# Kernel optimization log

Measured on AMD Instinct MI355X. Metric: run time of the kernel, lower is better.

Reference implementation:

```python
import jax, jax.numpy as jnp
import numpy as np
from jax import lax


def setup_inputs() -> dict:
    key = jax.random.key(0)
    k1, k2, k3, k4, k5 = jax.random.split(key, 5)
    B, T, K = 512, 1024, 64
    emissions = jax.random.normal(k1, (B, T, K), dtype=jnp.float32)
    tags = jax.random.randint(k2, (B, T), 0, K).astype(jnp.int64)
    mask = jnp.ones((B, T), dtype=bool)
    # CRF parameters, init uniform(-0.1, 0.1) as in reset_parameters
    transitions = jax.random.uniform(k3, (K, K), minval=-0.1, maxval=0.1, dtype=jnp.float32)
    start_transitions = jax.random.uniform(k4, (K,), minval=-0.1, maxval=0.1, dtype=jnp.float32)
    end_transitions = jax.random.uniform(k5, (K,), minval=-0.1, maxval=0.1, dtype=jnp.float32)
    return {"emissions": emissions, "tags": tags, "mask": mask,
            "transitions": transitions, "start_transitions": start_transitions,
            "end_transitions": end_transitions}


def _log_partition(em, mk, transitions, start_transitions, end_transitions):
    # em: (T, B, K) time-major; mk: (T, B) bool
    def step(score, inp):
        em_t, m_t = inp                     # (B, K), (B,)
        # (B, K_prev, 1) + (K_prev, K_next) + (B, 1, K_next) -> lse over prev
        nxt = jax.nn.logsumexp(score[:, :, None] + transitions[None, :, :]
                               + em_t[:, None, :], axis=1)
        score = jnp.where(m_t[:, None], nxt, score)
        return score, None
    score0 = start_transitions + em[0]      # (B, K)
    score, _ = lax.scan(step, score0, (em[1:], mk[1:]))
    return jax.nn.logsumexp(score + end_transitions, axis=1)  # (B,)


def _gold_score(em, tg, mk, transitions, start_transitions, end_transitions):
    # em: (T, B, K); tg: (T, B) int; mk: (T, B) bool
    T, B, K = em.shape
    mf = mk.astype(em.dtype)
    emis = jnp.take_along_axis(em, tg[:, :, None], axis=2)[:, :, 0]  # (T, B)
    score = start_transitions[tg[0]] + jnp.sum(emis * mf, axis=0)
    trans = transitions[tg[:-1], tg[1:]]                              # (T-1, B)
    score = score + jnp.sum(trans * mf[1:], axis=0)
    last_idx = jnp.sum(mk, axis=0).astype(jnp.int32) - 1
    last_tags = tg[last_idx, jnp.arange(B)]
    return score + end_transitions[last_tags]


def reference(emissions, tags, mask, transitions, start_transitions, end_transitions):
    # batch_first=True -> transpose to time-major (T, B, ...)
    em = jnp.transpose(emissions, (1, 0, 2))
    tg = tags.T
    mk = mask.T
    logZ = _log_partition(em, mk, transitions, start_transitions, end_transitions)
    gold = _gold_score(em, tg, mk, transitions, start_transitions, end_transitions)
    return jnp.mean(logZ - gold)
```

## Files before the change

kernel.cpp:

```cpp
#include <hip/hip_runtime.h>
#include <hip/hip_bf16.h>

#define TT 1024
#define KS 64
#define PFD 8

typedef __attribute__((ext_vector_type(8))) short bf16x8;
typedef __attribute__((ext_vector_type(4))) float f32x4;

__device__ __forceinline__ unsigned short f2bf(float x) {
    union { __hip_bfloat16 h; unsigned short s; } u;
    u.h = __float2bfloat16(x);
    return u.s;
}
__device__ __forceinline__ float bflo(unsigned u) {
    union { unsigned v; float f; } w; w.v = u << 16; return w.f;
}
__device__ __forceinline__ float bfhi(unsigned u) {
    union { unsigned v; float f; } w; w.v = u & 0xFFFF0000u; return w.f;
}
__device__ __forceinline__ unsigned cvtpk(float a, float b) {
    unsigned r;
    asm("v_cvt_pk_bf16_f32 %0, %1, %2" : "=v"(r) : "v"(a), "v"(b));
    return r;
}
__device__ __forceinline__ unsigned pkadd(unsigned a, unsigned b) {
    unsigned r;
    asm("v_pk_add_u16 %0, %1, %2" : "=v"(r) : "v"(a), "v"(b));
    return r;
}

__global__ __launch_bounds__(256) void crf_expem(
    const float* __restrict__ em, uint4* __restrict__ g, long long n8)
{
    long long i = (long long)blockIdx.x * blockDim.x + threadIdx.x;
    const long long stride = (long long)gridDim.x * blockDim.x;
    const float4* p = (const float4*)em;
    for (; i < n8; i += stride) {
        float4 a = p[i * 2], b = p[i * 2 + 1];
        uint4 o;
        o.x = (unsigned)f2bf(__expf(a.x)) | ((unsigned)f2bf(__expf(a.y)) << 16);
        o.y = (unsigned)f2bf(__expf(a.z)) | ((unsigned)f2bf(__expf(a.w)) << 16);
        o.z = (unsigned)f2bf(__expf(b.x)) | ((unsigned)f2bf(__expf(b.y)) << 16);
        o.w = (unsigned)f2bf(__expf(b.z)) | ((unsigned)f2bf(__expf(b.w)) << 16);
        g[i] = o;
    }
}

__global__ __launch_bounds__(64, 1) void crf_logZ_v11(
    const float* __restrict__ em,
    const uint4* __restrict__ g4,
    const int* __restrict__ mask,
    const float* __restrict__ trans,
    const float* __restrict__ startT,
    const float* __restrict__ endT,
    float* __restrict__ logZ)
{
    const int l = threadIdx.x;
    const int c = l & 15;
    const int h = l >> 4;
    const long long b = (long long)blockIdx.x * 16 + c;

    const int sigc = 8 * (c >> 2) + (c & 3);
    bf16x8 E[4][2];
#pragma unroll
    for (int m = 0; m < 4; ++m) {
        const int col = 32 * (m >> 1) + 4 * (m & 1) + sigc;
#pragma unroll
        for (int kk = 0; kk < 2; ++kk) {
            union { unsigned short s[8]; bf16x8 v; } u;
#pragma unroll
            for (int e = 0; e < 8; ++e)
                u.s[e] = f2bf(__expf(trans[(32 * kk + 8 * h + e) * KS + col]));
            E[m][kk] = u.v;
        }
    }

    const long long embase = b * (long long)TT * KS;
    const unsigned long long gp =
        (unsigned long long)(const void*)((const char*)g4 + embase * 2 + h * 16);
    const unsigned long long mp =
        (unsigned long long)(const void*)(mask + b * TT);

    unsigned aw0, aw1, aw2, aw3, aw4, aw5, aw6, aw7;
    {
        const float* erow = em + embase;
        float w0[16];
#pragma unroll
        for (int kk = 0; kk < 2; ++kk)
#pragma unroll
            for (int e = 0; e < 8; ++e) {
                const int j = 32 * kk + 8 * h + e;
                w0[8 * kk + e] = __expf(erow[j] + startT[j]);
            }
        aw0 = cvtpk(w0[0], w0[1]);   aw1 = cvtpk(w0[2], w0[3]);
        aw2 = cvtpk(w0[4], w0[5]);   aw3 = cvtpk(w0[6], w0[7]);
        aw4 = cvtpk(w0[8], w0[9]);   aw5 = cvtpk(w0[10], w0[11]);
        aw6 = cvtpk(w0[12], w0[13]); aw7 = cvtpk(w0[14], w0[15]);
    }
    float M = 0.f;

    uint4 ga[PFD], gc[PFD];
    int   mvp[PFD];
#pragma unroll
    for (int u = 0; u < PFD; ++u) {
        const unsigned long long a  = gp + (unsigned long long)(1 + u) * 128ull;
        const unsigned long long ma = mp + (unsigned long long)(1 + u) * 4ull;
        asm volatile("global_load_dwordx4 %0, %1, off" : "=&v"(ga[u]) : "v"(a));
        asm volatile("global_load_dwordx4 %0, %1, off offset:64" : "=&v"(gc[u]) : "v"(a));
        asm volatile("global_load_dword %0, %1, off" : "=&v"(mvp[u]) : "v"(ma));
    }

    unsigned kadd = 0;
    float    sln2 = 0.f;
#define CRF_CTRL() do {                                                        \
    const unsigned l0 = aw0 & 0xffffu, h0 = aw0 >> 16;                         \
    const unsigned l4 = aw4 & 0xffffu, h4 = aw4 >> 16;                         \
    unsigned um = l0 > h0 ? l0 : h0;                                           \
    um = um > l4 ? um : l4;  um = um > h4 ? um : h4;                           \
    unsigned sx = (unsigned)__shfl_xor((int)um, 16); um = um > sx ? um : sx;   \
    sx = (unsigned)__shfl_xor((int)um, 32);          um = um > sx ? um : sx;   \
    const unsigned k16 = (0x3F80u - (um & 0x7F80u)) & 0xffffu;                 \
    kadd = (k16 << 16) | k16;                                                  \
    sln2 = (float)((int)((um >> 7) & 0xffu) - 127) * 0.693147180559945f;       \
} while (0)

#define CRF_STEP(t, u, APPLY) do {                                             \
    union { unsigned uu[4]; bf16x8 v; } A0, A1;                                \
    A0.uu[0] = aw0; A0.uu[1] = aw1; A0.uu[2] = aw2; A0.uu[3] = aw3;            \
    A1.uu[0] = aw4; A1.uu[1] = aw5; A1.uu[2] = aw6; A1.uu[3] = aw7;            \
    const f32x4 z = {0.f, 0.f, 0.f, 0.f};                                      \
    f32x4 d0 = __builtin_amdgcn_mfma_f32_16x16x32_bf16(E[0][0], A0.v, z,0,0,0);\
    f32x4 d1 = __builtin_amdgcn_mfma_f32_16x16x32_bf16(E[1][0], A0.v, z,0,0,0);\
    f32x4 d2 = __builtin_amdgcn_mfma_f32_16x16x32_bf16(E[2][0], A0.v, z,0,0,0);\
    f32x4 d3 = __builtin_amdgcn_mfma_f32_16x16x32_bf16(E[3][0], A0.v, z,0,0,0);\
    d0 = __builtin_amdgcn_mfma_f32_16x16x32_bf16(E[0][1], A1.v, d0, 0,0,0);    \
    d1 = __builtin_amdgcn_mfma_f32_16x16x32_bf16(E[1][1], A1.v, d1, 0,0,0);    \
    d2 = __builtin_amdgcn_mfma_f32_16x16x32_bf16(E[2][1], A1.v, d2, 0,0,0);    \
    d3 = __builtin_amdgcn_mfma_f32_16x16x32_bf16(E[3][1], A1.v, d3, 0,0,0);    \
    asm volatile("s_waitcnt vmcnt(21)" ::: "memory");                          \
    __builtin_amdgcn_sched_barrier(0);                                         \
    const uint4 v0 = ga[u], v1 = gc[u];                                        \
    const int mvv = ((t) <= TT - 1) ? mvp[u] : 0;                              \
    const float g00 = bflo(v0.x), g01 = bfhi(v0.x);                            \
    const float g02 = bflo(v0.y), g03 = bfhi(v0.y);                            \
    const float g10 = bflo(v0.z), g11 = bfhi(v0.z);                            \
    const float g12 = bflo(v0.w), g13 = bfhi(v0.w);                            \
    const float g20 = bflo(v1.x), g21 = bfhi(v1.x);                            \
    const float g22 = bflo(v1.y), g23 = bfhi(v1.y);                            \
    const float g30 = bflo(v1.z), g31 = bfhi(v1.z);                            \
    const float g32 = bflo(v1.w), g33 = bfhi(v1.w);                            \
    unsigned q0, q1, q2, q3, q4, q5, q6, q7;                                   \
    if (APPLY) {                                                               \
        q0 = pkadd(cvtpk(d0.x * g00, d0.y * g01), kadd);                       \
        q1 = pkadd(cvtpk(d0.z * g02, d0.w * g03), kadd);                       \
        q2 = pkadd(cvtpk(d1.x * g10, d1.y * g11), kadd);                       \
        q3 = pkadd(cvtpk(d1.z * g12, d1.w * g13), kadd);                       \
        q4 = pkadd(cvtpk(d2.x * g20, d2.y * g21), kadd);                       \
        q5 = pkadd(cvtpk(d2.z * g22, d2.w * g23), kadd);                       \
        q6 = pkadd(cvtpk(d3.x * g30, d3.y * g31), kadd);                       \
        q7 = pkadd(cvtpk(d3.z * g32, d3.w * g33), kadd);                       \
    } else {                                                                   \
        q0 = cvtpk(d0.x * g00, d0.y * g01);                                    \
        q1 = cvtpk(d0.z * g02, d0.w * g03);                                    \
        q2 = cvtpk(d1.x * g10, d1.y * g11);                                    \
        q3 = cvtpk(d1.z * g12, d1.w * g13);                                    \
        q4 = cvtpk(d2.x * g20, d2.y * g21);                                    \
        q5 = cvtpk(d2.z * g22, d2.w * g23);                                    \
        q6 = cvtpk(d3.x * g30, d3.y * g31);                                    \
        q7 = cvtpk(d3.z * g32, d3.w * g33);                                    \
    }                                                                          \
    aw0 = mvv ? q0 : aw0; aw1 = mvv ? q1 : aw1;                                \
    aw2 = mvv ? q2 : aw2; aw3 = mvv ? q3 : aw3;                                \
    aw4 = mvv ? q4 : aw4; aw5 = mvv ? q5 : aw5;                                \
    aw6 = mvv ? q6 : aw6; aw7 = mvv ? q7 : aw7;                                \
    if (APPLY) { M = mvv ? (M + sln2) : M; }                                   \
    {                                                                          \
        const int tn = ((t) + PFD <= TT - 1) ? ((t) + PFD) : (TT - 1);         \
        const unsigned long long a  = gp + (unsigned long long)tn * 128ull;    \
        const unsigned long long ma = mp + (unsigned long long)tn * 4ull;      \
        asm volatile("global_load_dwordx4 %0, %1, off" : "=&v"(ga[u]) : "v"(a)); \
        asm volatile("global_load_dwordx4 %0, %1, off offset:64" : "=&v"(gc[u]) : "v"(a)); \
        asm volatile("global_load_dword %0, %1, off" : "=&v"(mvp[u]) : "v"(ma)); \
    }                                                                          \
} while (0)

    for (int t0 = 1; t0 < TT + 1; t0 += PFD) {
        CRF_STEP(t0 + 0, 0, 0);
        CRF_CTRL();
        CRF_STEP(t0 + 1, 1, 0);
        CRF_STEP(t0 + 2, 2, 1);
        CRF_STEP(t0 + 3, 3, 0);
        CRF_STEP(t0 + 4, 4, 0);
        CRF_CTRL();
        CRF_STEP(t0 + 5, 5, 0);
        CRF_STEP(t0 + 6, 6, 1);
        CRF_STEP(t0 + 7, 7, 0);
    }
#undef CRF_STEP
#undef CRF_CTRL

    float val = 0.f;
    {
        const unsigned a[8] = {aw0, aw1, aw2, aw3, aw4, aw5, aw6, aw7};
#pragma unroll
        for (int kk = 0; kk < 2; ++kk)
#pragma unroll
            for (int wi = 0; wi < 4; ++wi) {
                const int j0 = 32 * kk + 8 * h + 2 * wi;
                const unsigned wq = a[4 * kk + wi];
                val += bflo(wq) * __expf(endT[j0]);
                val += bfhi(wq) * __expf(endT[j0 + 1]);
            }
    }
    val += __shfl_xor(val, 16);
    val += __shfl_xor(val, 32);
    if (l < 16) logZ[(long long)blockIdx.x * 16 + l] = M + __logf(val);
}

__global__ __launch_bounds__(64, 1) void crf_logZ_fb(
    const float* __restrict__ em, const int* __restrict__ mask,
    const float* __restrict__ trans, const float* __restrict__ startT,
    const float* __restrict__ endT, float* __restrict__ logZ)
{
    const int l = threadIdx.x;
    const int c = l & 15;
    const int h = l >> 4;
    const long long b = (long long)blockIdx.x * 16 + c;

    const int sigc = 8 * (c >> 2) + (c & 3);
    bf16x8 E[4][2];
#pragma unroll
    for (int m = 0; m < 4; ++m) {
        const int col = 32 * (m >> 1) + 4 * (m & 1) + sigc;
#pragma unroll
        for (int kk = 0; kk < 2; ++kk) {
            union { unsigned short s[8]; bf16x8 v; } u;
#pragma unroll
            for (int e = 0; e < 8; ++e)
                u.s[e] = f2bf(__expf(trans[(32 * kk + 8 * h + e) * KS + col]));
            E[m][kk] = u.v;
        }
    }
    const long long embase = b * (long long)TT * KS;
    const int* mrow = mask + b * TT;
    const float* erow = em + embase;

    unsigned aw[8];
    {
        float w0[16];
#pragma unroll
        for (int kk = 0; kk < 2; ++kk)
#pragma unroll
            for (int e = 0; e < 8; ++e) {
                const int j = 32 * kk + 8 * h + e;
                w0[8 * kk + e] = __expf(erow[j] + startT[j]);
            }
#pragma unroll
        for (int i = 0; i < 8; ++i) aw[i] = cvtpk(w0[2 * i], w0[2 * i + 1]);
    }
    float M = 0.f;

    for (int t = 1; t < TT; ++t) {
        union { unsigned uu[4]; bf16x8 v; } A0, A1;
#pragma unroll
        for (int i = 0; i < 4; ++i) { A0.uu[i] = aw[i]; A1.uu[i] = aw[4 + i]; }
        const f32x4 z = {0.f, 0.f, 0.f, 0.f};
        f32x4 d0 = __builtin_amdgcn_mfma_f32_16x16x32_bf16(E[0][0], A0.v, z,0,0,0);
        f32x4 d1 = __builtin_amdgcn_mfma_f32_16x16x32_bf16(E[1][0], A0.v, z,0,0,0);
        f32x4 d2 = __builtin_amdgcn_mfma_f32_16x16x32_bf16(E[2][0], A0.v, z,0,0,0);
        f32x4 d3 = __builtin_amdgcn_mfma_f32_16x16x32_bf16(E[3][0], A0.v, z,0,0,0);
        d0 = __builtin_amdgcn_mfma_f32_16x16x32_bf16(E[0][1], A1.v, d0, 0,0,0);
        d1 = __builtin_amdgcn_mfma_f32_16x16x32_bf16(E[1][1], A1.v, d1, 0,0,0);
        d2 = __builtin_amdgcn_mfma_f32_16x16x32_bf16(E[2][1], A1.v, d2, 0,0,0);
        d3 = __builtin_amdgcn_mfma_f32_16x16x32_bf16(E[3][1], A1.v, d3, 0,0,0);
        const float r0 = __shfl(d0.x, c);
        float gf[16];
#pragma unroll
        for (int kk = 0; kk < 2; ++kk)
#pragma unroll
            for (int e = 0; e < 8; ++e)
                gf[8 * kk + e] = __expf(erow[(long long)t * KS + 32 * kk + 8 * h + e]);
        const int sh = 127 - (int)((__float_as_uint(r0) >> 23) & 0xff);
        const unsigned k16 = (unsigned)(unsigned short)(sh * 128);
        const unsigned kadd = (k16 << 16) | k16;
        const int mv = mrow[t];
        const f32x4 dd[4] = {d0, d1, d2, d3};
#pragma unroll
        for (int i = 0; i < 8; ++i) {
            const f32x4 dv = dd[i >> 1];
            const float x = (i & 1) ? dv.z : dv.x;
            const float y = (i & 1) ? dv.w : dv.y;
            const unsigned q = pkadd(cvtpk(x * gf[2 * i], y * gf[2 * i + 1]), kadd);
            aw[i] = mv ? q : aw[i];
        }
        M = mv ? (M - (float)sh * 0.693147180559945f) : M;
    }

    float val = 0.f;
#pragma unroll
    for (int kk = 0; kk < 2; ++kk)
#pragma unroll
        for (int wi = 0; wi < 4; ++wi) {
            const int j0 = 32 * kk + 8 * h + 2 * wi;
            const unsigned wq = aw[4 * kk + wi];
            val += bflo(wq) * __expf(endT[j0]);
            val += bfhi(wq) * __expf(endT[j0 + 1]);
        }
    val += __shfl_xor(val, 16);
    val += __shfl_xor(val, 32);
    if (l < 16) logZ[(long long)blockIdx.x * 16 + l] = M + __logf(val);
}

__global__ __launch_bounds__(256) void crf_gold_kernel(
    const float* __restrict__ em, const int* __restrict__ tags,
    const int* __restrict__ mask, const float* __restrict__ trans,
    const float* __restrict__ startT, const float* __restrict__ endT,
    float* __restrict__ gold, int T)
{
    const int b = blockIdx.x;
    const int tid = threadIdx.x;
    const float* emb = em + (size_t)b * T * KS;
    const int* tb = tags + (size_t)b * T;
    const int* mb = mask + (size_t)b * T;

    float acc = 0.f;
    int cnt = 0;
    for (int t = tid; t < T; t += 256) {
        int tg = tb[t];
        int mv = mb[t];
        float mf = mv ? 1.f : 0.f;
        acc += emb[t * KS + tg] * mf;
        if (t >= 1) acc += trans[tb[t - 1] * KS + tg] * mf;
        cnt += mv ? 1 : 0;
    }
#pragma unroll
    for (int off = 32; off; off >>= 1) {
        acc += __shfl_xor(acc, off);
        cnt += __shfl_xor(cnt, off);
    }
    __shared__ float wacc[4];
    __shared__ int   wcnt[4];
    int wv = tid >> 6;
    if ((tid & 63) == 0) { wacc[wv] = acc; wcnt[wv] = cnt; }
    __syncthreads();
    if (tid == 0) {
        float a = wacc[0] + wacc[1] + wacc[2] + wacc[3];
        int   cc = wcnt[0] + wcnt[1] + wcnt[2] + wcnt[3];
        gold[b] = a + startT[tb[0]] + endT[tb[cc - 1]];
    }
}

__global__ __launch_bounds__(512) void crf_reduce_kernel(
    const float* __restrict__ logZ, const float* __restrict__ gold,
    float* __restrict__ out, int B)
{
    int tid = threadIdx.x;
    float v = 0.f;
    for (int i = tid; i < B; i += 512) v += logZ[i] - gold[i];
#pragma unroll
    for (int off = 32; off; off >>= 1) v += __shfl_xor(v, off);
    __shared__ float ws[8];
    int w = tid >> 6;
    if ((tid & 63) == 0) ws[w] = v;
    __syncthreads();
    if (tid == 0) {
        float s = 0.f;
#pragma unroll
        for (int k = 0; k < 8; ++k) s += ws[k];
        out[0] = s / (float)B;
    }
}

extern "C" void kernel_launch(void* const* d_in, const int* in_sizes, int n_in,
                              void* d_out, int out_size, void* d_ws, size_t ws_size,
                              hipStream_t stream)
{
    const float* emissions = (const float*)d_in[0];
    const int*   tags      = (const int*)d_in[1];
    const int*   mask      = (const int*)d_in[2];
    const float* trans     = (const float*)d_in[3];
    const float* startT    = (const float*)d_in[4];
    const float* endT      = (const float*)d_in[5];

    const int T = TT;
    const int B = in_sizes[1] / T;

    float* logZ = (float*)d_ws;
    float* gold = logZ + B;

    const size_t gbytes = (size_t)B * T * KS * 2;
    const bool pre = (ws_size >= 4096 + gbytes) && (B % 16 == 0);

    if (pre) {
        uint4* g = (uint4*)((char*)d_ws + 4096);
        long long n8 = (long long)B * T * KS / 8;
        crf_expem<<<2048, 256, 0, stream>>>(emissions, g, n8);
        crf_logZ_v11<<<B / 16, 64, 0, stream>>>(
            emissions, (const uint4*)g, mask, trans, startT, endT, logZ);
    } else {
        crf_logZ_fb<<<B / 16, 64, 0, stream>>>(
            emissions, mask, trans, startT, endT, logZ);
    }
    crf_gold_kernel<<<B, 256, 0, stream>>>(emissions, tags, mask, trans, startT, endT, gold, T);
    crf_reduce_kernel<<<1, 512, 0, stream>>>(logZ, gold, (float*)d_out, B);
}
```

Measured before the change: 262.3 us.

## Fuse gold-score into logZ launch and stage exp(emissions) as fp32

```diff
diff --git a/kernel.cpp b/kernel.cpp
--- a/kernel.cpp
+++ b/kernel.cpp
@@ -3,10 +3,11 @@
 
 #define TT 1024
 #define KS 64
-#define PFD 8
+#define PFD 4
 
 typedef __attribute__((ext_vector_type(8))) short bf16x8;
 typedef __attribute__((ext_vector_type(4))) float f32x4;
+typedef __attribute__((ext_vector_type(2))) float f32x2;
 
 __device__ __forceinline__ unsigned short f2bf(float x) {
     union { __hip_bfloat16 h; unsigned short s; } u;
@@ -29,33 +30,80 @@
     asm("v_pk_add_u16 %0, %1, %2" : "=v"(r) : "v"(a), "v"(b));
     return r;
 }
-
-__global__ __launch_bounds__(256) void crf_expem(
-    const float* __restrict__ em, uint4* __restrict__ g, long long n8)
+__device__ __forceinline__ f32x2 pkmul(f32x2 a, f32x2 b) {
+    f32x2 r;
+    asm("v_pk_mul_f32 %0, %1, %2" : "=v"(r) : "v"(a), "v"(b));
+    return r;
+}
+__device__ __forceinline__ f32x2 lo2(f32x4 v) { return __builtin_shufflevector(v, v, 0, 1); }
+__device__ __forceinline__ f32x2 hi2(f32x4 v) { return __builtin_shufflevector(v, v, 2, 3); }
+
+__global__ __launch_bounds__(256) void crf_expem_f32(
+    const float* __restrict__ em, float4* __restrict__ g, long long n4)
 {
     long long i = (long long)blockIdx.x * blockDim.x + threadIdx.x;
     const long long stride = (long long)gridDim.x * blockDim.x;
     const float4* p = (const float4*)em;
-    for (; i < n8; i += stride) {
-        float4 a = p[i * 2], b = p[i * 2 + 1];
-        uint4 o;
-        o.x = (unsigned)f2bf(__expf(a.x)) | ((unsigned)f2bf(__expf(a.y)) << 16);
-        o.y = (unsigned)f2bf(__expf(a.z)) | ((unsigned)f2bf(__expf(a.w)) << 16);
-        o.z = (unsigned)f2bf(__expf(b.x)) | ((unsigned)f2bf(__expf(b.y)) << 16);
-        o.w = (unsigned)f2bf(__expf(b.z)) | ((unsigned)f2bf(__expf(b.w)) << 16);
+    for (; i < n4; i += stride) {
+        float4 a = p[i];
+        float4 o;
+        o.x = __expf(a.x); o.y = __expf(a.y);
+        o.z = __expf(a.z); o.w = __expf(a.w);
         g[i] = o;
     }
 }
 
-__global__ __launch_bounds__(64, 1) void crf_logZ_v11(
+__global__ __launch_bounds__(256, 1) void crf_fused(
     const float* __restrict__ em,
-    const uint4* __restrict__ g4,
+    const float* __restrict__ gf,
     const int* __restrict__ mask,
+    const int* __restrict__ tags,
     const float* __restrict__ trans,
     const float* __restrict__ startT,
     const float* __restrict__ endT,
-    float* __restrict__ logZ)
-{
+    float* __restrict__ logZ,
+    float* __restrict__ gold,
+    int nZ)
+{
+    __shared__ float wacc[4];
+    __shared__ int   wcnt[4];
+
+    if ((int)blockIdx.x >= nZ) {
+        const int b = (int)blockIdx.x - nZ;
+        const int tid = threadIdx.x;
+        const float* emb = em + (size_t)b * TT * KS;
+        const int* tb = tags + (size_t)b * TT;
+        const int* mb = mask + (size_t)b * TT;
+
+        float acc = 0.f;
+        int cnt = 0;
+        for (int t = tid; t < TT; t += 256) {
+            int tg = tb[t];
+            int mv = mb[t];
+            float mf = mv ? 1.f : 0.f;
+            acc += emb[t * KS + tg] * mf;
+            if (t >= 1) acc += trans[tb[t - 1] * KS + tg] * mf;
+            cnt += mv ? 1 : 0;
+        }
+#pragma unroll
+        for (int off = 32; off; off >>= 1) {
+            acc += __shfl_xor(acc, off);
+            cnt += __shfl_xor(cnt, off);
+        }
+        int wv = tid >> 6;
+        if ((tid & 63) == 0) { wacc[wv] = acc; wcnt[wv] = cnt; }
+        __syncthreads();
+        if (tid == 0) {
+            float a = wacc[0] + wacc[1] + wacc[2] + wacc[3];
+            int   cc = wcnt[0] + wcnt[1] + wcnt[2] + wcnt[3];
+            gold[b] = a + startT[tb[0]] + endT[tb[cc - 1]];
+        }
+        return;
+    }
+
+    if (threadIdx.x >= 64) return;
+    __builtin_amdgcn_s_setprio(1);
+
     const int l = threadIdx.x;
     const int c = l & 15;
     const int h = l >> 4;
@@ -78,7 +126,7 @@
 
     const long long embase = b * (long long)TT * KS;
     const unsigned long long gp =
-        (unsigned long long)(const void*)((const char*)g4 + embase * 2 + h * 16);
+        (unsigned long long)(const void*)((const char*)gf + embase * 4 + h * 32);
     const unsigned long long mp =
         (unsigned long long)(const void*)(mask + b * TT);
 
@@ -100,14 +148,16 @@
     }
     float M = 0.f;
 
-    uint4 ga[PFD], gc[PFD];
+    f32x4 gA[PFD], gB[PFD], gC[PFD], gD[PFD];
     int   mvp[PFD];
 #pragma unroll
     for (int u = 0; u < PFD; ++u) {
-        const unsigned long long a  = gp + (unsigned long long)(1 + u) * 128ull;
+        const unsigned long long a  = gp + (unsigned long long)(1 + u) * 256ull;
         const unsigned long long ma = mp + (unsigned long long)(1 + u) * 4ull;
-        asm volatile("global_load_dwordx4 %0, %1, off" : "=&v"(ga[u]) : "v"(a));
-        asm volatile("global_load_dwordx4 %0, %1, off offset:64" : "=&v"(gc[u]) : "v"(a));
+        asm volatile("global_load_dwordx4 %0, %1, off" : "=&v"(gA[u]) : "v"(a));
+        asm volatile("global_load_dwordx4 %0, %1, off offset:16" : "=&v"(gB[u]) : "v"(a));
+        asm volatile("global_load_dwordx4 %0, %1, off offset:128" : "=&v"(gC[u]) : "v"(a));
+        asm volatile("global_load_dwordx4 %0, %1, off offset:144" : "=&v"(gD[u]) : "v"(a));
         asm volatile("global_load_dword %0, %1, off" : "=&v"(mvp[u]) : "v"(ma));
     }
 
@@ -138,37 +188,33 @@
     d1 = __builtin_amdgcn_mfma_f32_16x16x32_bf16(E[1][1], A1.v, d1, 0,0,0);    \
     d2 = __builtin_amdgcn_mfma_f32_16x16x32_bf16(E[2][1], A1.v, d2, 0,0,0);    \
     d3 = __builtin_amdgcn_mfma_f32_16x16x32_bf16(E[3][1], A1.v, d3, 0,0,0);    \
-    asm volatile("s_waitcnt vmcnt(21)" ::: "memory");                          \
+    asm volatile("s_waitcnt vmcnt(15)" ::: "memory");                          \
     __builtin_amdgcn_sched_barrier(0);                                         \
-    const uint4 v0 = ga[u], v1 = gc[u];                                        \
+    const f32x4 v0 = gA[u], v1 = gB[u], v2 = gC[u], v3 = gD[u];                \
     const int mvv = ((t) <= TT - 1) ? mvp[u] : 0;                              \
-    const float g00 = bflo(v0.x), g01 = bfhi(v0.x);                            \
-    const float g02 = bflo(v0.y), g03 = bfhi(v0.y);                            \
-    const float g10 = bflo(v0.z), g11 = bfhi(v0.z);                            \
-    const float g12 = bflo(v0.w), g13 = bfhi(v0.w);                            \
-    const float g20 = bflo(v1.x), g21 = bfhi(v1.x);                            \
-    const float g22 = bflo(v1.y), g23 = bfhi(v1.y);                            \
-    const float g30 = bflo(v1.z), g31 = bfhi(v1.z);                            \
-    const float g32 = bflo(v1.w), g33 = bfhi(v1.w);                            \
+    const f32x2 p0 = pkmul(lo2(d0), lo2(v0));                                  \
+    const f32x2 p1 = pkmul(hi2(d0), hi2(v0));                                  \
+    const f32x2 p2 = pkmul(lo2(d1), lo2(v1));                                  \
+    const f32x2 p3 = pkmul(hi2(d1), hi2(v1));                                  \
+    const f32x2 p4 = pkmul(lo2(d2), lo2(v2));                                  \
+    const f32x2 p5 = pkmul(hi2(d2), hi2(v2));                                  \
+    const f32x2 p6 = pkmul(lo2(d3), lo2(v3));                                  \
+    const f32x2 p7 = pkmul(hi2(d3), hi2(v3));                                  \
     unsigned q0, q1, q2, q3, q4, q5, q6, q7;                                   \
     if (APPLY) {                                                               \
-        q0 = pkadd(cvtpk(d0.x * g00, d0.y * g01), kadd);                       \
-        q1 = pkadd(cvtpk(d0.z * g02, d0.w * g03), kadd);                       \
-        q2 = pkadd(cvtpk(d1.x * g10, d1.y * g11), kadd);                       \
-        q3 = pkadd(cvtpk(d1.z * g12, d1.w * g13), kadd);                       \
-        q4 = pkadd(cvtpk(d2.x * g20, d2.y * g21), kadd);                       \
-        q5 = pkadd(cvtpk(d2.z * g22, d2.w * g23), kadd);                       \
-        q6 = pkadd(cvtpk(d3.x * g30, d3.y * g31), kadd);                       \
-        q7 = pkadd(cvtpk(d3.z * g32, d3.w * g33), kadd);                       \
+        q0 = pkadd(cvtpk(p0[0], p0[1]), kadd);                                 \
+        q1 = pkadd(cvtpk(p1[0], p1[1]), kadd);                                 \
+        q2 = pkadd(cvtpk(p2[0], p2[1]), kadd);                                 \
+        q3 = pkadd(cvtpk(p3[0], p3[1]), kadd);                                 \
+        q4 = pkadd(cvtpk(p4[0], p4[1]), kadd);                                 \
+        q5 = pkadd(cvtpk(p5[0], p5[1]), kadd);                                 \
+        q6 = pkadd(cvtpk(p6[0], p6[1]), kadd);                                 \
+        q7 = pkadd(cvtpk(p7[0], p7[1]), kadd);                                 \
     } else {                                                                   \
-        q0 = cvtpk(d0.x * g00, d0.y * g01);                                    \
-        q1 = cvtpk(d0.z * g02, d0.w * g03);                                    \
-        q2 = cvtpk(d1.x * g10, d1.y * g11);                                    \
-        q3 = cvtpk(d1.z * g12, d1.w * g13);                                    \
-        q4 = cvtpk(d2.x * g20, d2.y * g21);                                    \
-        q5 = cvtpk(d2.z * g22, d2.w * g23);                                    \
-        q6 = cvtpk(d3.x * g30, d3.y * g31);                                    \
-        q7 = cvtpk(d3.z * g32, d3.w * g33);                                    \
+        q0 = cvtpk(p0[0], p0[1]);  q1 = cvtpk(p1[0], p1[1]);                   \
+        q2 = cvtpk(p2[0], p2[1]);  q3 = cvtpk(p3[0], p3[1]);                   \
+        q4 = cvtpk(p4[0], p4[1]);  q5 = cvtpk(p5[0], p5[1]);                   \
+        q6 = cvtpk(p6[0], p6[1]);  q7 = cvtpk(p7[0], p7[1]);                   \
     }                                                                          \
     aw0 = mvv ? q0 : aw0; aw1 = mvv ? q1 : aw1;                                \
     aw2 = mvv ? q2 : aw2; aw3 = mvv ? q3 : aw3;                                \
@@ -177,10 +223,12 @@
     if (APPLY) { M = mvv ? (M + sln2) : M; }                                   \
     {                                                                          \
         const int tn = ((t) + PFD <= TT - 1) ? ((t) + PFD) : (TT - 1);         \
-        const unsigned long long a  = gp + (unsigned long long)tn * 128ull;    \
+        const unsigned long long a  = gp + (unsigned long long)tn * 256ull;    \
         const unsigned long long ma = mp + (unsigned long long)tn * 4ull;      \
-        asm volatile("global_load_dwordx4 %0, %1, off" : "=&v"(ga[u]) : "v"(a)); \
-        asm volatile("global_load_dwordx4 %0, %1, off offset:64" : "=&v"(gc[u]) : "v"(a)); \
+        asm volatile("global_load_dwordx4 %0, %1, off" : "=&v"(gA[u]) : "v"(a)); \
+        asm volatile("global_load_dwordx4 %0, %1, off offset:16" : "=&v"(gB[u]) : "v"(a)); \
+        asm volatile("global_load_dwordx4 %0, %1, off offset:128" : "=&v"(gC[u]) : "v"(a)); \
+        asm volatile("global_load_dwordx4 %0, %1, off offset:144" : "=&v"(gD[u]) : "v"(a)); \
         asm volatile("global_load_dword %0, %1, off" : "=&v"(mvp[u]) : "v"(ma)); \
     }                                                                          \
 } while (0)
@@ -191,14 +239,10 @@
         CRF_STEP(t0 + 1, 1, 0);
         CRF_STEP(t0 + 2, 2, 1);
         CRF_STEP(t0 + 3, 3, 0);
-        CRF_STEP(t0 + 4, 4, 0);
-        CRF_CTRL();
-        CRF_STEP(t0 + 5, 5, 0);
-        CRF_STEP(t0 + 6, 6, 1);
-        CRF_STEP(t0 + 7, 7, 0);
     }
 #undef CRF_STEP
 #undef CRF_CTRL
+    __builtin_amdgcn_s_setprio(0);
 
     float val = 0.f;
     {
@@ -389,19 +433,21 @@
     float* logZ = (float*)d_ws;
     float* gold = logZ + B;
 
-    const size_t gbytes = (size_t)B * T * KS * 2;
-    const bool pre = (ws_size >= 4096 + gbytes) && (B % 16 == 0);
-
-    if (pre) {
-        uint4* g = (uint4*)((char*)d_ws + 4096);
-        long long n8 = (long long)B * T * KS / 8;
-        crf_expem<<<2048, 256, 0, stream>>>(emissions, g, n8);
-        crf_logZ_v11<<<B / 16, 64, 0, stream>>>(
-            emissions, (const uint4*)g, mask, trans, startT, endT, logZ);
+    const size_t g32 = (size_t)B * T * KS * 4;
+
+    if (ws_size >= 8192 + g32 && (B % 16) == 0) {
+        float4* g = (float4*)((char*)d_ws + 8192);
+        const int nZ = B / 16;
+        crf_expem_f32<<<2048, 256, 0, stream>>>(
+            emissions, g, (long long)B * T * KS / 4);
+        crf_fused<<<nZ + B, 256, 0, stream>>>(
+            emissions, (const float*)g, mask, tags, trans, startT, endT,
+            logZ, gold, nZ);
     } else {
         crf_logZ_fb<<<B / 16, 64, 0, stream>>>(
             emissions, mask, trans, startT, endT, logZ);
-    }
-    crf_gold_kernel<<<B, 256, 0, stream>>>(emissions, tags, mask, trans, startT, endT, gold, T);
+        crf_gold_kernel<<<B, 256, 0, stream>>>(
+            emissions, tags, mask, trans, startT, endT, gold, T);
+    }
     crf_reduce_kernel<<<1, 512, 0, stream>>>(logZ, gold, (float*)d_out, B);
 }
```

After: 241.6 us. 1.09x faster.

## Interleave two batch groups per wave and fuse gold-score into logZ launch

Applied to the files above, without the earlier changes.

```diff
diff --git a/kernel.cpp b/kernel.cpp
--- a/kernel.cpp
+++ b/kernel.cpp
@@ -3,7 +3,6 @@
 
 #define TT 1024
 #define KS 64
-#define PFD 8
 
 typedef __attribute__((ext_vector_type(8))) short bf16x8;
 typedef __attribute__((ext_vector_type(4))) float f32x4;
@@ -30,7 +29,7 @@
     return r;
 }
 
-__global__ __launch_bounds__(256) void crf_expem(
+__global__ __launch_bounds__(256) void crf_expem_bf16(
     const float* __restrict__ em, uint4* __restrict__ g, long long n8)
 {
     long long i = (long long)blockIdx.x * blockDim.x + threadIdx.x;
@@ -47,19 +46,62 @@
     }
 }
 
-__global__ __launch_bounds__(64, 1) void crf_logZ_v11(
+__global__ __launch_bounds__(256, 1) void crf_fused2(
     const float* __restrict__ em,
     const uint4* __restrict__ g4,
     const int* __restrict__ mask,
+    const int* __restrict__ tags,
     const float* __restrict__ trans,
     const float* __restrict__ startT,
     const float* __restrict__ endT,
-    float* __restrict__ logZ)
+    float* __restrict__ logZ,
+    float* __restrict__ gold,
+    int nZ)
 {
+    __shared__ float wacc[4];
+    __shared__ int   wcnt[4];
+
+    if ((int)blockIdx.x >= nZ) {
+        const int b = (int)blockIdx.x - nZ;
+        const int tid = threadIdx.x;
+        const float* emb = em + (size_t)b * TT * KS;
+        const int* tb = tags + (size_t)b * TT;
+        const int* mb = mask + (size_t)b * TT;
+
+        float acc = 0.f;
+        int cnt = 0;
+        for (int t = tid; t < TT; t += 256) {
+            int tg = tb[t];
+            int mv = mb[t];
+            float mf = mv ? 1.f : 0.f;
+            acc += emb[t * KS + tg] * mf;
+            if (t >= 1) acc += trans[tb[t - 1] * KS + tg] * mf;
+            cnt += mv ? 1 : 0;
+        }
+#pragma unroll
+        for (int off = 32; off; off >>= 1) {
+            acc += __shfl_xor(acc, off);
+            cnt += __shfl_xor(cnt, off);
+        }
+        int wv = tid >> 6;
+        if ((tid & 63) == 0) { wacc[wv] = acc; wcnt[wv] = cnt; }
+        __syncthreads();
+        if (tid == 0) {
+            float a = wacc[0] + wacc[1] + wacc[2] + wacc[3];
+            int   cc = wcnt[0] + wcnt[1] + wcnt[2] + wcnt[3];
+            gold[b] = a + startT[tb[0]] + endT[tb[cc - 1]];
+        }
+        return;
+    }
+
+    if (threadIdx.x >= 64) return;
+    __builtin_amdgcn_s_setprio(1);
+
     const int l = threadIdx.x;
     const int c = l & 15;
     const int h = l >> 4;
-    const long long b = (long long)blockIdx.x * 16 + c;
+    const long long bA = (long long)blockIdx.x * 32 + c;
+    const long long bB = bA + 16;
 
     const int sigc = 8 * (c >> 2) + (c & 3);
     bf16x8 E[4][2];
@@ -76,72 +118,85 @@
         }
     }
 
-    const long long embase = b * (long long)TT * KS;
-    const unsigned long long gp =
-        (unsigned long long)(const void*)((const char*)g4 + embase * 2 + h * 16);
-    const unsigned long long mp =
-        (unsigned long long)(const void*)(mask + b * TT);
-
-    unsigned aw0, aw1, aw2, aw3, aw4, aw5, aw6, aw7;
+    const long long embA = bA * (long long)TT * KS;
+    const long long embB = bB * (long long)TT * KS;
+    const unsigned long long gpA =
+        (unsigned long long)(const void*)((const char*)g4 + embA * 2 + h * 16);
+    const unsigned long long gpB =
+        (unsigned long long)(const void*)((const char*)g4 + embB * 2 + h * 16);
+    const unsigned long long mpA =
+        (unsigned long long)(const void*)(mask + bA * TT);
+    const unsigned long long mpB =
+        (unsigned long long)(const void*)(mask + bB * TT);
+
+    unsigned awA0, awA1, awA2, awA3, awA4, awA5, awA6, awA7;
+    unsigned awB0, awB1, awB2, awB3, awB4, awB5, awB6, awB7;
     {
-        const float* erow = em + embase;
-        float w0[16];
+        const float* erA = em + embA;
+        const float* erB = em + embB;
+        float wa[16], wb[16];
 #pragma unroll
         for (int kk = 0; kk < 2; ++kk)
 #pragma unroll
             for (int e = 0; e < 8; ++e) {
                 const int j = 32 * kk + 8 * h + e;
-                w0[8 * kk + e] = __expf(erow[j] + startT[j]);
+                wa[8 * kk + e] = __expf(erA[j] + startT[j]);
+                wb[8 * kk + e] = __expf(erB[j] + startT[j]);
             }
-        aw0 = cvtpk(w0[0], w0[1]);   aw1 = cvtpk(w0[2], w0[3]);
-        aw2 = cvtpk(w0[4], w0[5]);   aw3 = cvtpk(w0[6], w0[7]);
-        aw4 = cvtpk(w0[8], w0[9]);   aw5 = cvtpk(w0[10], w0[11]);
-        aw6 = cvtpk(w0[12], w0[13]); aw7 = cvtpk(w0[14], w0[15]);
-    }
-    float M = 0.f;
-
-    uint4 ga[PFD], gc[PFD];
-    int   mvp[PFD];
-#pragma unroll
-    for (int u = 0; u < PFD; ++u) {
-        const unsigned long long a  = gp + (unsigned long long)(1 + u) * 128ull;
-        const unsigned long long ma = mp + (unsigned long long)(1 + u) * 4ull;
-        asm volatile("global_load_dwordx4 %0, %1, off" : "=&v"(ga[u]) : "v"(a));
-        asm volatile("global_load_dwordx4 %0, %1, off offset:64" : "=&v"(gc[u]) : "v"(a));
-        asm volatile("global_load_dword %0, %1, off" : "=&v"(mvp[u]) : "v"(ma));
-    }
-
-    unsigned kadd = 0;
-    float    sln2 = 0.f;
-#define CRF_CTRL() do {                                                        \
-    const unsigned l0 = aw0 & 0xffffu, h0 = aw0 >> 16;                         \
-    const unsigned l4 = aw4 & 0xffffu, h4 = aw4 >> 16;                         \
+        awA0 = cvtpk(wa[0], wa[1]);   awA1 = cvtpk(wa[2], wa[3]);
+        awA2 = cvtpk(wa[4], wa[5]);   awA3 = cvtpk(wa[6], wa[7]);
+        awA4 = cvtpk(wa[8], wa[9]);   awA5 = cvtpk(wa[10], wa[11]);
+        awA6 = cvtpk(wa[12], wa[13]); awA7 = cvtpk(wa[14], wa[15]);
+        awB0 = cvtpk(wb[0], wb[1]);   awB1 = cvtpk(wb[2], wb[3]);
+        awB2 = cvtpk(wb[4], wb[5]);   awB3 = cvtpk(wb[6], wb[7]);
+        awB4 = cvtpk(wb[8], wb[9]);   awB5 = cvtpk(wb[10], wb[11]);
+        awB6 = cvtpk(wb[12], wb[13]); awB7 = cvtpk(wb[14], wb[15]);
+    }
+    float MA = 0.f, MB = 0.f;
+
+    uint4 gaA[2], gcA[2], gaB[2], gcB[2];
+    int   mvA[2], mvB[2];
+#pragma unroll
+    for (int u = 0; u < 2; ++u) {
+        const unsigned long long aa = gpA + (unsigned long long)(1 + u) * 128ull;
+        const unsigned long long ab = gpB + (unsigned long long)(1 + u) * 128ull;
+        const unsigned long long ma = mpA + (unsigned long long)(1 + u) * 4ull;
+        const unsigned long long mb = mpB + (unsigned long long)(1 + u) * 4ull;
+        asm volatile("global_load_dwordx4 %0, %1, off" : "=&v"(gaA[u]) : "v"(aa));
+        asm volatile("global_load_dwordx4 %0, %1, off offset:64" : "=&v"(gcA[u]) : "v"(aa));
+        asm volatile("global_load_dword %0, %1, off" : "=&v"(mvA[u]) : "v"(ma));
+        asm volatile("global_load_dwordx4 %0, %1, off" : "=&v"(gaB[u]) : "v"(ab));
+        asm volatile("global_load_dwordx4 %0, %1, off offset:64" : "=&v"(gcB[u]) : "v"(ab));
+        asm volatile("global_load_dword %0, %1, off" : "=&v"(mvB[u]) : "v"(mb));
+    }
+
+    unsigned kaddA = 0, kaddB = 0;
+    float sln2A = 0.f, sln2B = 0.f;
+
+#define CRF_CTRL(W0, W4, KADD, SLN2) do {                                      \
+    const unsigned l0 = (W0) & 0xffffu, h0 = (W0) >> 16;                       \
+    const unsigned l4 = (W4) & 0xffffu, h4 = (W4) >> 16;                       \
     unsigned um = l0 > h0 ? l0 : h0;                                           \
     um = um > l4 ? um : l4;  um = um > h4 ? um : h4;                           \
     unsigned sx = (unsigned)__shfl_xor((int)um, 16); um = um > sx ? um : sx;   \
     sx = (unsigned)__shfl_xor((int)um, 32);          um = um > sx ? um : sx;   \
     const unsigned k16 = (0x3F80u - (um & 0x7F80u)) & 0xffffu;                 \
-    kadd = (k16 << 16) | k16;                                                  \
-    sln2 = (float)((int)((um >> 7) & 0xffu) - 127) * 0.693147180559945f;       \
+    KADD = (k16 << 16) | k16;                                                  \
+    SLN2 = (float)((int)((um >> 7) & 0xffu) - 127) * 0.693147180559945f;       \
 } while (0)
 
-#define CRF_STEP(t, u, APPLY) do {                                             \
-    union { unsigned uu[4]; bf16x8 v; } A0, A1;                                \
-    A0.uu[0] = aw0; A0.uu[1] = aw1; A0.uu[2] = aw2; A0.uu[3] = aw3;            \
-    A1.uu[0] = aw4; A1.uu[1] = aw5; A1.uu[2] = aw6; A1.uu[3] = aw7;            \
-    const f32x4 z = {0.f, 0.f, 0.f, 0.f};                                      \
-    f32x4 d0 = __builtin_amdgcn_mfma_f32_16x16x32_bf16(E[0][0], A0.v, z,0,0,0);\
-    f32x4 d1 = __builtin_amdgcn_mfma_f32_16x16x32_bf16(E[1][0], A0.v, z,0,0,0);\
-    f32x4 d2 = __builtin_amdgcn_mfma_f32_16x16x32_bf16(E[2][0], A0.v, z,0,0,0);\
-    f32x4 d3 = __builtin_amdgcn_mfma_f32_16x16x32_bf16(E[3][0], A0.v, z,0,0,0);\
-    d0 = __builtin_amdgcn_mfma_f32_16x16x32_bf16(E[0][1], A1.v, d0, 0,0,0);    \
-    d1 = __builtin_amdgcn_mfma_f32_16x16x32_bf16(E[1][1], A1.v, d1, 0,0,0);    \
-    d2 = __builtin_amdgcn_mfma_f32_16x16x32_bf16(E[2][1], A1.v, d2, 0,0,0);    \
-    d3 = __builtin_amdgcn_mfma_f32_16x16x32_bf16(E[3][1], A1.v, d3, 0,0,0);    \
-    asm volatile("s_waitcnt vmcnt(21)" ::: "memory");                          \
-    __builtin_amdgcn_sched_barrier(0);                                         \
-    const uint4 v0 = ga[u], v1 = gc[u];                                        \
-    const int mvv = ((t) <= TT - 1) ? mvp[u] : 0;                              \
+#define CRF_TAIL(SFX, t, u, APPLY, DOCTRL, GP, MP, d0, d1, d2, d3)             \
+do {                                                                           \
+    const uint4 v0 = ga##SFX[u], v1 = gc##SFX[u];                              \
+    const int mvv = ((t) <= TT - 1) ? mv##SFX[u] : 0;                          \
+    {                                                                          \
+        const int tn = ((t) + 2 <= TT - 1) ? ((t) + 2) : (TT - 1);             \
+        const unsigned long long a  = (GP) + (unsigned long long)tn * 128ull;  \
+        const unsigned long long ma = (MP) + (unsigned long long)tn * 4ull;    \
+        asm volatile("global_load_dwordx4 %0, %1, off" : "=&v"(ga##SFX[u]) : "v"(a)); \
+        asm volatile("global_load_dwordx4 %0, %1, off offset:64" : "=&v"(gc##SFX[u]) : "v"(a)); \
+        asm volatile("global_load_dword %0, %1, off" : "=&v"(mv##SFX[u]) : "v"(ma)); \
+    }                                                                          \
     const float g00 = bflo(v0.x), g01 = bfhi(v0.x);                            \
     const float g02 = bflo(v0.y), g03 = bfhi(v0.y);                            \
     const float g10 = bflo(v0.z), g11 = bfhi(v0.z);                            \
@@ -152,14 +207,14 @@
     const float g32 = bflo(v1.w), g33 = bfhi(v1.w);                            \
     unsigned q0, q1, q2, q3, q4, q5, q6, q7;                                   \
     if (APPLY) {                                                               \
-        q0 = pkadd(cvtpk(d0.x * g00, d0.y * g01), kadd);                       \
-        q1 = pkadd(cvtpk(d0.z * g02, d0.w * g03), kadd);                       \
-        q2 = pkadd(cvtpk(d1.x * g10, d1.y * g11), kadd);                       \
-        q3 = pkadd(cvtpk(d1.z * g12, d1.w * g13), kadd);                       \
-        q4 = pkadd(cvtpk(d2.x * g20, d2.y * g21), kadd);                       \
-        q5 = pkadd(cvtpk(d2.z * g22, d2.w * g23), kadd);                       \
-        q6 = pkadd(cvtpk(d3.x * g30, d3.y * g31), kadd);                       \
-        q7 = pkadd(cvtpk(d3.z * g32, d3.w * g33), kadd);                       \
+        q0 = pkadd(cvtpk(d0.x * g00, d0.y * g01), kadd##SFX);                  \
+        q1 = pkadd(cvtpk(d0.z * g02, d0.w * g03), kadd##SFX);                  \
+        q2 = pkadd(cvtpk(d1.x * g10, d1.y * g11), kadd##SFX);                  \
+        q3 = pkadd(cvtpk(d1.z * g12, d1.w * g13), kadd##SFX);                  \
+        q4 = pkadd(cvtpk(d2.x * g20, d2.y * g21), kadd##SFX);                  \
+        q5 = pkadd(cvtpk(d2.z * g22, d2.w * g23), kadd##SFX);                  \
+        q6 = pkadd(cvtpk(d3.x * g30, d3.y * g31), kadd##SFX);                  \
+        q7 = pkadd(cvtpk(d3.z * g32, d3.w * g33), kadd##SFX);                  \
     } else {                                                                   \
         q0 = cvtpk(d0.x * g00, d0.y * g01);                                    \
         q1 = cvtpk(d0.z * g02, d0.w * g03);                                    \
@@ -170,52 +225,89 @@
         q6 = cvtpk(d3.x * g30, d3.y * g31);                                    \
         q7 = cvtpk(d3.z * g32, d3.w * g33);                                    \
     }                                                                          \
-    aw0 = mvv ? q0 : aw0; aw1 = mvv ? q1 : aw1;                                \
-    aw2 = mvv ? q2 : aw2; aw3 = mvv ? q3 : aw3;                                \
-    aw4 = mvv ? q4 : aw4; aw5 = mvv ? q5 : aw5;                                \
-    aw6 = mvv ? q6 : aw6; aw7 = mvv ? q7 : aw7;                                \
-    if (APPLY) { M = mvv ? (M + sln2) : M; }                                   \
-    {                                                                          \
-        const int tn = ((t) + PFD <= TT - 1) ? ((t) + PFD) : (TT - 1);         \
-        const unsigned long long a  = gp + (unsigned long long)tn * 128ull;    \
-        const unsigned long long ma = mp + (unsigned long long)tn * 4ull;      \
-        asm volatile("global_load_dwordx4 %0, %1, off" : "=&v"(ga[u]) : "v"(a)); \
-        asm volatile("global_load_dwordx4 %0, %1, off offset:64" : "=&v"(gc[u]) : "v"(a)); \
-        asm volatile("global_load_dword %0, %1, off" : "=&v"(mvp[u]) : "v"(ma)); \
-    }                                                                          \
+    aw##SFX##0 = mvv ? q0 : aw##SFX##0; aw##SFX##1 = mvv ? q1 : aw##SFX##1;    \
+    aw##SFX##2 = mvv ? q2 : aw##SFX##2; aw##SFX##3 = mvv ? q3 : aw##SFX##3;    \
+    aw##SFX##4 = mvv ? q4 : aw##SFX##4; aw##SFX##5 = mvv ? q5 : aw##SFX##5;    \
+    aw##SFX##6 = mvv ? q6 : aw##SFX##6; aw##SFX##7 = mvv ? q7 : aw##SFX##7;    \
+    if (APPLY) { M##SFX = mvv ? (M##SFX + sln2##SFX) : M##SFX; }               \
+    if (DOCTRL) CRF_CTRL(aw##SFX##0, aw##SFX##4, kadd##SFX, sln2##SFX);        \
 } while (0)
 
-    for (int t0 = 1; t0 < TT + 1; t0 += PFD) {
-        CRF_STEP(t0 + 0, 0, 0);
-        CRF_CTRL();
-        CRF_STEP(t0 + 1, 1, 0);
-        CRF_STEP(t0 + 2, 2, 1);
-        CRF_STEP(t0 + 3, 3, 0);
-        CRF_STEP(t0 + 4, 4, 0);
-        CRF_CTRL();
-        CRF_STEP(t0 + 5, 5, 0);
-        CRF_STEP(t0 + 6, 6, 1);
-        CRF_STEP(t0 + 7, 7, 0);
-    }
-#undef CRF_STEP
+#define CRF_DSTEP(t, u, APPLY, DOCTRL) do {                                    \
+    union { unsigned uu[4]; bf16x8 v; } Aa0, Aa1, Ba0, Ba1;                    \
+    Aa0.uu[0] = awA0; Aa0.uu[1] = awA1; Aa0.uu[2] = awA2; Aa0.uu[3] = awA3;    \
+    Aa1.uu[0] = awA4; Aa1.uu[1] = awA5; Aa1.uu[2] = awA6; Aa1.uu[3] = awA7;    \
+    Ba0.uu[0] = awB0; Ba0.uu[1] = awB1; Ba0.uu[2] = awB2; Ba0.uu[3] = awB3;    \
+    Ba1.uu[0] = awB4; Ba1.uu[1] = awB5; Ba1.uu[2] = awB6; Ba1.uu[3] = awB7;    \
+    const f32x4 z = {0.f, 0.f, 0.f, 0.f};                                      \
+    f32x4 dA0 = __builtin_amdgcn_mfma_f32_16x16x32_bf16(E[0][0], Aa0.v, z,0,0,0); \
+    f32x4 dA1 = __builtin_amdgcn_mfma_f32_16x16x32_bf16(E[1][0], Aa0.v, z,0,0,0); \
+    f32x4 dA2 = __builtin_amdgcn_mfma_f32_16x16x32_bf16(E[2][0], Aa0.v, z,0,0,0); \
+    f32x4 dA3 = __builtin_amdgcn_mfma_f32_16x16x32_bf16(E[3][0], Aa0.v, z,0,0,0); \
+    dA0 = __builtin_amdgcn_mfma_f32_16x16x32_bf16(E[0][1], Aa1.v, dA0, 0,0,0); \
+    dA1 = __builtin_amdgcn_mfma_f32_16x16x32_bf16(E[1][1], Aa1.v, dA1, 0,0,0); \
+    dA2 = __builtin_amdgcn_mfma_f32_16x16x32_bf16(E[2][1], Aa1.v, dA2, 0,0,0); \
+    dA3 = __builtin_amdgcn_mfma_f32_16x16x32_bf16(E[3][1], Aa1.v, dA3, 0,0,0); \
+    f32x4 dB0 = __builtin_amdgcn_mfma_f32_16x16x32_bf16(E[0][0], Ba0.v, z,0,0,0); \
+    f32x4 dB1 = __builtin_amdgcn_mfma_f32_16x16x32_bf16(E[1][0], Ba0.v, z,0,0,0); \
+    f32x4 dB2 = __builtin_amdgcn_mfma_f32_16x16x32_bf16(E[2][0], Ba0.v, z,0,0,0); \
+    f32x4 dB3 = __builtin_amdgcn_mfma_f32_16x16x32_bf16(E[3][0], Ba0.v, z,0,0,0); \
+    dB0 = __builtin_amdgcn_mfma_f32_16x16x32_bf16(E[0][1], Ba1.v, dB0, 0,0,0); \
+    dB1 = __builtin_amdgcn_mfma_f32_16x16x32_bf16(E[1][1], Ba1.v, dB1, 0,0,0); \
+    dB2 = __builtin_amdgcn_mfma_f32_16x16x32_bf16(E[2][1], Ba1.v, dB2, 0,0,0); \
+    dB3 = __builtin_amdgcn_mfma_f32_16x16x32_bf16(E[3][1], Ba1.v, dB3, 0,0,0); \
+    asm volatile("s_waitcnt vmcnt(9)" ::: "memory");                           \
+    __builtin_amdgcn_sched_barrier(0);                                         \
+    CRF_TAIL(A, t, u, APPLY, DOCTRL, gpA, mpA, dA0, dA1, dA2, dA3);            \
+    asm volatile("s_waitcnt vmcnt(9)" ::: "memory");                           \
+    __builtin_amdgcn_sched_barrier(0);                                         \
+    CRF_TAIL(B, t, u, APPLY, DOCTRL, gpB, mpB, dB0, dB1, dB2, dB3);            \
+} while (0)
+
+    for (int t0 = 1; t0 < TT + 1; t0 += 4) {
+        CRF_DSTEP(t0 + 0, 0, 0, 1);
+        CRF_DSTEP(t0 + 1, 1, 0, 0);
+        CRF_DSTEP(t0 + 2, 0, 1, 0);
+        CRF_DSTEP(t0 + 3, 1, 0, 0);
+    }
+#undef CRF_DSTEP
+#undef CRF_TAIL
 #undef CRF_CTRL
-
-    float val = 0.f;
+    __builtin_amdgcn_s_setprio(0);
+
+    float endE[16];
+#pragma unroll
+    for (int kk = 0; kk < 2; ++kk)
+#pragma unroll
+        for (int wi = 0; wi < 4; ++wi) {
+            const int j0 = 32 * kk + 8 * h + 2 * wi;
+            endE[8 * kk + 2 * wi] = __expf(endT[j0]);
+            endE[8 * kk + 2 * wi + 1] = __expf(endT[j0 + 1]);
+        }
+    float valA = 0.f, valB = 0.f;
     {
-        const unsigned a[8] = {aw0, aw1, aw2, aw3, aw4, aw5, aw6, aw7};
+        const unsigned aA[8] = {awA0, awA1, awA2, awA3, awA4, awA5, awA6, awA7};
+        const unsigned aB[8] = {awB0, awB1, awB2, awB3, awB4, awB5, awB6, awB7};
 #pragma unroll
         for (int kk = 0; kk < 2; ++kk)
 #pragma unroll
             for (int wi = 0; wi < 4; ++wi) {
-                const int j0 = 32 * kk + 8 * h + 2 * wi;
-                const unsigned wq = a[4 * kk + wi];
-                val += bflo(wq) * __expf(endT[j0]);
-                val += bfhi(wq) * __expf(endT[j0 + 1]);
+                const unsigned wqA = aA[4 * kk + wi];
+                const unsigned wqB = aB[4 * kk + wi];
+                valA += bflo(wqA) * endE[8 * kk + 2 * wi];
+                valA += bfhi(wqA) * endE[8 * kk + 2 * wi + 1];
+                valB += bflo(wqB) * endE[8 * kk + 2 * wi];
+                valB += bfhi(wqB) * endE[8 * kk + 2 * wi + 1];
             }
     }
-    val += __shfl_xor(val, 16);
-    val += __shfl_xor(val, 32);
-    if (l < 16) logZ[(long long)blockIdx.x * 16 + l] = M + __logf(val);
+    valA += __shfl_xor(valA, 16);
+    valA += __shfl_xor(valA, 32);
+    valB += __shfl_xor(valB, 16);
+    valB += __shfl_xor(valB, 32);
+    if (l < 16) {
+        logZ[(long long)blockIdx.x * 32 + l]      = MA + __logf(valA);
+        logZ[(long long)blockIdx.x * 32 + 16 + l] = MB + __logf(valB);
+    }
 }
 
 __global__ __launch_bounds__(64, 1) void crf_logZ_fb(
@@ -389,19 +481,21 @@
     float* logZ = (float*)d_ws;
     float* gold = logZ + B;
 
-    const size_t gbytes = (size_t)B * T * KS * 2;
-    const bool pre = (ws_size >= 4096 + gbytes) && (B % 16 == 0);
-
-    if (pre) {
-        uint4* g = (uint4*)((char*)d_ws + 4096);
-        long long n8 = (long long)B * T * KS / 8;
-        crf_expem<<<2048, 256, 0, stream>>>(emissions, g, n8);
-        crf_logZ_v11<<<B / 16, 64, 0, stream>>>(
-            emissions, (const uint4*)g, mask, trans, startT, endT, logZ);
+    const size_t g16 = (size_t)B * T * KS * 2;
+
+    if (ws_size >= 8192 + g16 && (B % 32) == 0) {
+        uint4* g = (uint4*)((char*)d_ws + 8192);
+        const int nZ = B / 32;
+        crf_expem_bf16<<<2048, 256, 0, stream>>>(
+            emissions, g, (long long)B * T * KS / 8);
+        crf_fused2<<<nZ + B, 256, 0, stream>>>(
+            emissions, (const uint4*)g, mask, tags, trans, startT, endT,
+            logZ, gold, nZ);
     } else {
-        crf_logZ_fb<<<B / 16, 64, 0, stream>>>(
+        crf_logZ_fb<<<(B + 15) / 16, 64, 0, stream>>>(
             emissions, mask, trans, startT, endT, logZ);
-    }
-    crf_gold_kernel<<<B, 256, 0, stream>>>(emissions, tags, mask, trans, startT, endT, gold, T);
+        crf_gold_kernel<<<B, 256, 0, stream>>>(
+            emissions, tags, mask, trans, startT, endT, gold, T);
+    }
     crf_reduce_kernel<<<1, 512, 0, stream>>>(logZ, gold, (float*)d_out, B);
 }
```

After: 441.9 us (median of 2 runs). 68.5% more time.
